# Performance work log

Measured on AMD Instinct MI355X. Metric: run time of the kernel, lower is better.

## Reference

```python
import jax, jax.numpy as jnp
import numpy as np

# Model dims
B, S, D = 4, 2048, 2048   # batch, seq, emb_dim
E, K, M = 8, 2, 1024      # num_experts, num_experts_per_tok, intermediate_dim


def setup_inputs() -> dict:
    key = jax.random.key(0)
    k0, k1, k2, k3, k4 = jax.random.split(key, 5)
    d_scale = D ** -0.5
    m_scale = M ** -0.5
    return {
        "x": jax.random.normal(k0, (B, S, D), jnp.float32),
        "w_gate": jax.random.normal(k1, (D, E), jnp.float32) * d_scale,
        "wi_0": jax.random.normal(k2, (E, D, M), jnp.float32) * d_scale,  # gate proj per expert
        "wi_1": jax.random.normal(k3, (E, D, M), jnp.float32) * d_scale,  # up proj per expert
        "wo": jax.random.normal(k4, (E, M, D), jnp.float32) * m_scale,    # down proj per expert
    }


def reference(x, w_gate, wi_0, wi_1, wo):
    b, s, d = x.shape
    e = w_gate.shape[1]
    xf = x.reshape(-1, d)                       # [T, D], T = B*S
    # --- gate logits + top-k routing ---
    logits = jnp.dot(xf, w_gate)                # [T, E]
    top_logits, top_idx = jax.lax.top_k(logits, K)    # [T, K]
    weights = jax.nn.softmax(top_logits, axis=-1)     # [T, K] router weights
    # --- sort token copies by assigned expert (dispatch) ---
    flat_idx = top_idx.reshape(-1)              # [T*K] expert id per token copy
    sort_order = jnp.argsort(flat_idx)          # [T*K] dispatch permutation
    token_ids = sort_order // K                 # source token for each sorted slot
    sorted_x = jnp.take(xf, token_ids, axis=0)  # [T*K, D] gathered activations
    group_sizes = jnp.bincount(flat_idx, length=E).astype(jnp.int32)  # tokens per expert
    # --- grouped expert GEMMs (silu-gated MLP) ---
    h0 = jax.lax.ragged_dot(sorted_x, wi_0, group_sizes)  # [T*K, M]
    h1 = jax.lax.ragged_dot(sorted_x, wi_1, group_sizes)  # [T*K, M]
    inter = jax.nn.silu(h0) * h1
    out_sorted = jax.lax.ragged_dot(inter, wo, group_sizes)  # [T*K, D]
    # --- unsort + weighted combine ---
    unsort = jnp.argsort(sort_order)
    out = jnp.take(out_sorted, unsort, axis=0).reshape(-1, K, d)  # [T, K, D]
    out = jnp.einsum("tkd,tk->td", out, weights)
    return out.reshape(b, s, d)
```

## Files before the change

### kernel.cpp

```cpp
#include <hip/hip_runtime.h>
#include <hip/hip_bf16.h>
#include <math.h>

#define T_TOK 8192
#define DIM   2048
#define NE    8
#define MDIM  1024
#define TK    16384
#define CAP   (TK + 128)
#define MAXTILES 136

typedef __attribute__((ext_vector_type(8))) short bf16x8;
typedef __attribute__((ext_vector_type(4))) float f32x4;

typedef __attribute__((address_space(3))) unsigned char* lds_ptr_t;
typedef const __attribute__((address_space(1))) unsigned char* glb_ptr_t;

__device__ __forceinline__ unsigned short f2bf(float f) {
  union { float f; unsigned u; } v; v.f = f;
  unsigned r = v.u + 0x7fffu + ((v.u >> 16) & 1u);
  return (unsigned short)(r >> 16);
}

__device__ __forceinline__ void gload_lds16(const void* g, void* l) {
  __builtin_amdgcn_global_load_lds((glb_ptr_t)g, (lds_ptr_t)l, 16, 0, 0);
}

__global__ __launch_bounds__(256) void router_kernel(
    const float* __restrict__ x, const float* __restrict__ wg,
    int* __restrict__ tok_eid, float* __restrict__ tok_w) {
  __shared__ float wgT[NE][1024];
  int tid = threadIdx.x;
  int wave = tid >> 6, lane = tid & 63;
  int t0 = blockIdx.x * 16 + wave * 4;

  double acc[4][NE];
#pragma unroll
  for (int tt = 0; tt < 4; tt++)
#pragma unroll
    for (int e = 0; e < NE; e++) acc[tt][e] = 0.0;

  for (int p = 0; p < 2; p++) {
    __syncthreads();
#pragma unroll
    for (int j = tid; j < 2048; j += 256) {
      float4 v = ((const float4*)wg)[p * 2048 + j];
      int d = j >> 1, h = (j & 1) * 4;
      wgT[h + 0][d] = v.x;
      wgT[h + 1][d] = v.y;
      wgT[h + 2][d] = v.z;
      wgT[h + 3][d] = v.w;
    }
    __syncthreads();
#pragma unroll
    for (int it = 0; it < 4; it++) {
      int dd = it * 256 + lane * 4;
      int gd = p * 1024 + dd;
      float4 wf[NE];
#pragma unroll
      for (int e = 0; e < NE; e++) wf[e] = *(const float4*)&wgT[e][dd];
#pragma unroll
      for (int tt = 0; tt < 4; tt++) {
        float4 xv = *(const float4*)(x + (size_t)(t0 + tt) * DIM + gd);
#pragma unroll
        for (int e = 0; e < NE; e++) {
          acc[tt][e] += (double)xv.x * (double)wf[e].x;
          acc[tt][e] += (double)xv.y * (double)wf[e].y;
          acc[tt][e] += (double)xv.z * (double)wf[e].z;
          acc[tt][e] += (double)xv.w * (double)wf[e].w;
        }
      }
    }
  }
#pragma unroll
  for (int tt = 0; tt < 4; tt++)
#pragma unroll
    for (int e = 0; e < NE; e++) {
      double v = acc[tt][e];
#pragma unroll
      for (int off = 32; off > 0; off >>= 1) v += __shfl_down(v, off, 64);
      acc[tt][e] = v;
    }
  if (lane == 0) {
#pragma unroll
    for (int tt = 0; tt < 4; tt++) {
      int t = t0 + tt;
      int b0 = 0; double l0 = acc[tt][0];
#pragma unroll
      for (int e = 1; e < NE; e++) { if (acc[tt][e] > l0) { l0 = acc[tt][e]; b0 = e; } }
      int b1 = -1; double l1 = -1.0e300;
#pragma unroll
      for (int e = 0; e < NE; e++) { if (e != b0 && acc[tt][e] > l1) { l1 = acc[tt][e]; b1 = e; } }
      double w0 = 1.0 / (1.0 + exp(l1 - l0));
      tok_eid[2 * t]     = b0;
      tok_eid[2 * t + 1] = b1;
      tok_w[2 * t]     = (float)w0;
      tok_w[2 * t + 1] = (float)(1.0 - w0);
    }
  }
}

__global__ __launch_bounds__(256) void plan_kernel(
    const int* __restrict__ tok_eid, int* __restrict__ offsets,
    int* __restrict__ tstart, int* __restrict__ tok_slot) {
  __shared__ int cnt[256][NE];
  __shared__ int pre[256][NE];
  __shared__ int tot[NE];
  __shared__ int off_sh[NE + 1];
  int th = threadIdx.x;
  int c[NE];
#pragma unroll
  for (int k = 0; k < NE; k++) c[k] = 0;
  for (int i = 0; i < TK / 256; i++) {
    int e = tok_eid[i * 256 + th];
#pragma unroll
    for (int k = 0; k < NE; k++) c[k] += (e == k) ? 1 : 0;
  }
#pragma unroll
  for (int k = 0; k < NE; k++) cnt[th][k] = c[k];
  __syncthreads();
  if (th < NE) {
    int run = 0;
#pragma unroll 4
    for (int i = 0; i < 256; i++) { pre[i][th] = run; run += cnt[i][th]; }
    tot[th] = run;
  }
  __syncthreads();
  if (th == 0) {
    int s = 0, ts = 0;
    for (int e = 0; e < NE; e++) {
      off_sh[e] = s; offsets[e] = s; s += tot[e];
      tstart[e] = ts; ts += (tot[e] + 127) / 128;
    }
    offsets[NE] = s; off_sh[NE] = s; tstart[NE] = ts;
  }
  __syncthreads();
  int b[NE];
#pragma unroll
  for (int k = 0; k < NE; k++) b[k] = off_sh[k] + pre[th][k];
  for (int i = 0; i < TK / 256; i++) {
    int idx = i * 256 + th;
    int e = tok_eid[idx];
    int slot = 0;
#pragma unroll
    for (int k = 0; k < NE; k++) {
      slot = (e == k) ? b[k] : slot;
      b[k] += (e == k) ? 1 : 0;
    }
    tok_slot[idx] = slot;
  }
}

__global__ __launch_bounds__(256) void dispatch_kernel(
    const float* __restrict__ x, const int* __restrict__ tok_slot,
    unsigned short* __restrict__ sorted_x) {
  int t = blockIdx.x;
  size_t s0 = (size_t)tok_slot[2 * t] * DIM;
  size_t s1 = (size_t)tok_slot[2 * t + 1] * DIM;
  const float4* xr = (const float4*)(x + (size_t)t * DIM);
#pragma unroll
  for (int i = threadIdx.x; i < DIM / 4; i += 256) {
    float4 v = xr[i];
    ushort4 b;
    b.x = f2bf(v.x); b.y = f2bf(v.y); b.z = f2bf(v.z); b.w = f2bf(v.w);
    *(ushort4*)(sorted_x + s0 + (size_t)i * 4) = b;
    *(ushort4*)(sorted_x + s1 + (size_t)i * 4) = b;
  }
}

__global__ __launch_bounds__(256) void transpose_cast_kernel(
    const float* __restrict__ in, unsigned short* __restrict__ out, int R, int C) {
  __shared__ unsigned short tile[32][33];
  int e = blockIdx.z;
  const float* inp = in + (size_t)e * R * C;
  unsigned short* outp = out + (size_t)e * R * C;
  int c0 = blockIdx.x * 32, r0 = blockIdx.y * 32;
  int tx = threadIdx.x & 31, ty = threadIdx.x >> 5;
#pragma unroll
  for (int i = 0; i < 32; i += 8)
    tile[ty + i][tx] = f2bf(inp[(size_t)(r0 + ty + i) * C + (c0 + tx)]);
  __syncthreads();
#pragma unroll
  for (int i = 0; i < 32; i += 8)
    outp[(size_t)(c0 + ty + i) * R + (r0 + tx)] = tile[tx][ty + i];
}

__global__ __launch_bounds__(256) void gemm12_kernel(
    const unsigned short* __restrict__ A, const unsigned short* __restrict__ W0t,
    const unsigned short* __restrict__ W1t, const int* __restrict__ offsets,
    const int* __restrict__ tstart, unsigned short* __restrict__ inter) {
  int bx = blockIdx.x;
  if (bx >= tstart[NE]) return;
  int e = 0;
#pragma unroll
  for (int k = 1; k < NE; k++) if (tstart[k] <= bx) e = k;
  int row0 = offsets[e], row_end = offsets[e + 1];
  int tile_r0 = row0 + (bx - tstart[e]) * 128;
  if (tile_r0 >= row_end) return;
  int col0 = blockIdx.y * 64;

  __shared__ unsigned short As[128 * 32];
  __shared__ unsigned short B0s[64 * 32];
  __shared__ unsigned short B1s[64 * 32];

  int tid = threadIdx.x;
  int wave = tid >> 6, lane = tid & 63;
  int wm = wave >> 1, wn = wave & 1;

  const unsigned short* B0 = W0t + ((size_t)e * MDIM + col0) * DIM;
  const unsigned short* B1 = W1t + ((size_t)e * MDIM + col0) * DIM;

  f32x4 acc0[4][2], acc1[4][2];
#pragma unroll
  for (int i = 0; i < 4; i++)
#pragma unroll
    for (int j = 0; j < 2; j++) {
      acc0[i][j] = (f32x4){0.f, 0.f, 0.f, 0.f};
      acc1[i][j] = (f32x4){0.f, 0.f, 0.f, 0.f};
    }

  int lrow = lane >> 2;
  int lkoff = (lane & 3) * 8;

  for (int k0 = 0; k0 < DIM; k0 += 32) {
#pragma unroll
    for (int c = 0; c < 2; c++) {
      int r = wave * 32 + c * 16 + lrow;
      gload_lds16(A + (size_t)(tile_r0 + r) * DIM + k0 + lkoff,
                  &As[(wave * 32 + c * 16) * 32]);
    }
    {
      int r = wave * 16 + lrow;
      gload_lds16(B0 + (size_t)r * DIM + k0 + lkoff, &B0s[(wave * 16) * 32]);
      gload_lds16(B1 + (size_t)r * DIM + k0 + lkoff, &B1s[(wave * 16) * 32]);
    }
    __syncthreads();
    bf16x8 af[4], b0f[2], b1f[2];
#pragma unroll
    for (int mi = 0; mi < 4; mi++)
      af[mi] = *(const bf16x8*)&As[(wm * 64 + mi * 16 + (lane & 15)) * 32 + (lane >> 4) * 8];
#pragma unroll
    for (int ni = 0; ni < 2; ni++) {
      b0f[ni] = *(const bf16x8*)&B0s[(wn * 32 + ni * 16 + (lane & 15)) * 32 + (lane >> 4) * 8];
      b1f[ni] = *(const bf16x8*)&B1s[(wn * 32 + ni * 16 + (lane & 15)) * 32 + (lane >> 4) * 8];
    }
#pragma unroll
    for (int mi = 0; mi < 4; mi++)
#pragma unroll
      for (int ni = 0; ni < 2; ni++) {
        acc0[mi][ni] = __builtin_amdgcn_mfma_f32_16x16x32_bf16(af[mi], b0f[ni], acc0[mi][ni], 0, 0, 0);
        acc1[mi][ni] = __builtin_amdgcn_mfma_f32_16x16x32_bf16(af[mi], b1f[ni], acc1[mi][ni], 0, 0, 0);
      }
    __syncthreads();
  }
#pragma unroll
  for (int mi = 0; mi < 4; mi++)
#pragma unroll
    for (int reg = 0; reg < 4; reg++) {
      int grow = tile_r0 + wm * 64 + mi * 16 + (lane >> 4) * 4 + reg;
      if (grow < row_end) {
#pragma unroll
        for (int ni = 0; ni < 2; ni++) {
          float h0 = acc0[mi][ni][reg];
          float h1 = acc1[mi][ni][reg];
          float g = h0 / (1.0f + __expf(-h0));
          int col = col0 + wn * 32 + ni * 16 + (lane & 15);
          inter[(size_t)grow * MDIM + col] = f2bf(g * h1);
        }
      }
    }
}

__global__ __launch_bounds__(256) void gemm3_kernel(
    const unsigned short* __restrict__ A, const unsigned short* __restrict__ Wot,
    const int* __restrict__ offsets, const int* __restrict__ tstart,
    float* __restrict__ out_sorted) {
  int bx = blockIdx.x;
  if (bx >= tstart[NE]) return;
  int e = 0;
#pragma unroll
  for (int k = 1; k < NE; k++) if (tstart[k] <= bx) e = k;
  int row0 = offsets[e], row_end = offsets[e + 1];
  int tile_r0 = row0 + (bx - tstart[e]) * 128;
  if (tile_r0 >= row_end) return;
  int col0 = blockIdx.y * 128;

  __shared__ unsigned short As[128 * 32];
  __shared__ unsigned short Bs[128 * 32];

  int tid = threadIdx.x;
  int wave = tid >> 6, lane = tid & 63;
  int wm = wave >> 1, wn = wave & 1;

  const unsigned short* B = Wot + ((size_t)e * DIM + col0) * MDIM;

  f32x4 acc[4][4];
#pragma unroll
  for (int i = 0; i < 4; i++)
#pragma unroll
    for (int j = 0; j < 4; j++) acc[i][j] = (f32x4){0.f, 0.f, 0.f, 0.f};

  int lrow = lane >> 2;
  int lkoff = (lane & 3) * 8;

  for (int k0 = 0; k0 < MDIM; k0 += 32) {
#pragma unroll
    for (int c = 0; c < 2; c++) {
      int r = wave * 32 + c * 16 + lrow;
      gload_lds16(A + (size_t)(tile_r0 + r) * MDIM + k0 + lkoff,
                  &As[(wave * 32 + c * 16) * 32]);
      gload_lds16(B + (size_t)r * MDIM + k0 + lkoff,
                  &Bs[(wave * 32 + c * 16) * 32]);
    }
    __syncthreads();
    bf16x8 af[4], bfr[4];
#pragma unroll
    for (int mi = 0; mi < 4; mi++)
      af[mi] = *(const bf16x8*)&As[(wm * 64 + mi * 16 + (lane & 15)) * 32 + (lane >> 4) * 8];
#pragma unroll
    for (int ni = 0; ni < 4; ni++)
      bfr[ni] = *(const bf16x8*)&Bs[(wn * 64 + ni * 16 + (lane & 15)) * 32 + (lane >> 4) * 8];
#pragma unroll
    for (int mi = 0; mi < 4; mi++)
#pragma unroll
      for (int ni = 0; ni < 4; ni++)
        acc[mi][ni] = __builtin_amdgcn_mfma_f32_16x16x32_bf16(af[mi], bfr[ni], acc[mi][ni], 0, 0, 0);
    __syncthreads();
  }
#pragma unroll
  for (int mi = 0; mi < 4; mi++)
#pragma unroll
    for (int reg = 0; reg < 4; reg++) {
      int grow = tile_r0 + wm * 64 + mi * 16 + (lane >> 4) * 4 + reg;
      if (grow < row_end) {
        float* orow = out_sorted + (size_t)grow * DIM + col0 + wn * 64 + (lane & 15);
#pragma unroll
        for (int ni = 0; ni < 4; ni++)
          orow[ni * 16] = acc[mi][ni][reg];
      }
    }
}

__global__ __launch_bounds__(256) void combine_kernel(
    const float* __restrict__ os, const int* __restrict__ tok_slot,
    const float* __restrict__ tok_w, float* __restrict__ out) {
  int t = blockIdx.x * 4 + (threadIdx.x >> 6);
  int lane = threadIdx.x & 63;
  int s0 = tok_slot[2 * t], s1 = tok_slot[2 * t + 1];
  float w0 = tok_w[2 * t], w1 = tok_w[2 * t + 1];
  const float4* a = (const float4*)(os + (size_t)s0 * DIM);
  const float4* b = (const float4*)(os + (size_t)s1 * DIM);
  float4* o = (float4*)(out + (size_t)t * DIM);
#pragma unroll
  for (int i = lane; i < DIM / 4; i += 64) {
    float4 va = a[i], vb = b[i];
    float4 r;
    r.x = w0 * va.x + w1 * vb.x;
    r.y = w0 * va.y + w1 * vb.y;
    r.z = w0 * va.z + w1 * vb.z;
    r.w = w0 * va.w + w1 * vb.w;
    o[i] = r;
  }
}

extern "C" void kernel_launch(void* const* d_in, const int* in_sizes, int n_in,
                              void* d_out, int out_size, void* d_ws, size_t ws_size,
                              hipStream_t stream) {
  const float* x   = (const float*)d_in[0];
  const float* wg  = (const float*)d_in[1];
  const float* wi0 = (const float*)d_in[2];
  const float* wi1 = (const float*)d_in[3];
  const float* wo  = (const float*)d_in[4];
  float* out = (float*)d_out;

  char* ws = (char*)d_ws;
  size_t off = 0;
  auto alloc = [&](size_t bytes) -> void* {
    void* p = ws + off;
    off = (off + bytes + 255) & ~(size_t)255;
    return p;
  };
  int*   offsets  = (int*)alloc((NE + 1) * 4);
  int*   tstart   = (int*)alloc((NE + 1) * 4);
  int*   tok_eid  = (int*)alloc((size_t)2 * T_TOK * 4);
  float* tok_w    = (float*)alloc((size_t)2 * T_TOK * 4);
  int*   tok_slot = (int*)alloc((size_t)2 * T_TOK * 4);
  unsigned short* inter    = (unsigned short*)alloc((size_t)CAP * MDIM * 2);
  unsigned short* sorted_x = (unsigned short*)alloc((size_t)CAP * DIM * 2);
  unsigned short* W0t      = (unsigned short*)alloc((size_t)NE * MDIM * DIM * 2);
  unsigned short* W1t      = (unsigned short*)alloc((size_t)NE * MDIM * DIM * 2);
  unsigned short* Wot      = (unsigned short*)alloc((size_t)NE * DIM * MDIM * 2);
  float* out_sorted = (float*)sorted_x;

  router_kernel<<<T_TOK / 16, 256, 0, stream>>>(x, wg, tok_eid, tok_w);
  plan_kernel<<<1, 256, 0, stream>>>(tok_eid, offsets, tstart, tok_slot);
  dispatch_kernel<<<T_TOK, 256, 0, stream>>>(x, tok_slot, sorted_x);
  transpose_cast_kernel<<<dim3(MDIM / 32, DIM / 32, NE), 256, 0, stream>>>(wi0, W0t, DIM, MDIM);
  transpose_cast_kernel<<<dim3(MDIM / 32, DIM / 32, NE), 256, 0, stream>>>(wi1, W1t, DIM, MDIM);
  transpose_cast_kernel<<<dim3(DIM / 32, MDIM / 32, NE), 256, 0, stream>>>(wo, Wot, MDIM, DIM);

  gemm12_kernel<<<dim3(MAXTILES, MDIM / 64, 1), 256, 0, stream>>>(
      sorted_x, W0t, W1t, offsets, tstart, inter);
  gemm3_kernel<<<dim3(MAXTILES, DIM / 128, 1), 256, 0, stream>>>(
      inter, Wot, offsets, tstart, out_sorted);
  combine_kernel<<<T_TOK / 4, 256, 0, stream>>>(out_sorted, tok_slot, tok_w, out);
}
```

Before: 681.1 us.

## Rewrite grouped GEMMs with 256-row tiles, swizzled double-buffered LDS and interleaved loads

```diff
diff --git a/kernel.cpp b/kernel.cpp
--- a/kernel.cpp
+++ b/kernel.cpp
@@ -7,8 +7,8 @@
 #define NE    8
 #define MDIM  1024
 #define TK    16384
-#define CAP   (TK + 128)
-#define MAXTILES 136
+#define CAP   (TK + 256)
+#define MAXT  72
 
 typedef __attribute__((ext_vector_type(8))) short bf16x8;
 typedef __attribute__((ext_vector_type(4))) float f32x4;
@@ -24,6 +24,24 @@
 
 __device__ __forceinline__ void gload_lds16(const void* g, void* l) {
   __builtin_amdgcn_global_load_lds((glb_ptr_t)g, (lds_ptr_t)l, 16, 0, 0);
+}
+
+#define VM_FENCE(n) asm volatile("s_waitcnt vmcnt(" #n ")" ::: "memory")
+#define BARRIER() __builtin_amdgcn_s_barrier()
+
+__device__ __forceinline__ void stage_unit(const unsigned short* __restrict__ src,
+                                           int ld, unsigned char* lds, int tid) {
+#pragma unroll
+  for (int j = 0; j < 2; j++) {
+    int idx = j * 512 + tid;
+    int row = idx >> 3;
+    int gslot = (idx & 7) ^ (row & 7);
+    gload_lds16(src + (size_t)row * ld + gslot * 8, lds + ((idx & ~63) << 4));
+  }
+}
+
+__device__ __forceinline__ bf16x8 ldsfrag(const unsigned char* base, int row, int kb) {
+  return *(const bf16x8*)(base + row * 128 + (kb ^ ((row & 7) << 4)));
 }
 
 __global__ __launch_bounds__(256) void router_kernel(
@@ -130,7 +148,7 @@
     int s = 0, ts = 0;
     for (int e = 0; e < NE; e++) {
       off_sh[e] = s; offsets[e] = s; s += tot[e];
-      tstart[e] = ts; ts += (tot[e] + 127) / 128;
+      tstart[e] = ts; ts += (tot[e] + 255) / 256;
     }
     offsets[NE] = s; off_sh[NE] = s; tstart[NE] = ts;
   }
@@ -185,160 +203,284 @@
     outp[(size_t)(c0 + ty + i) * R + (r0 + tx)] = tile[tx][ty + i];
 }
 
-__global__ __launch_bounds__(256) void gemm12_kernel(
+__global__ __launch_bounds__(512, 2) void gemm12_kernel(
     const unsigned short* __restrict__ A, const unsigned short* __restrict__ W0t,
     const unsigned short* __restrict__ W1t, const int* __restrict__ offsets,
     const int* __restrict__ tstart, unsigned short* __restrict__ inter) {
+  extern __shared__ unsigned char smem[];
   int bx = blockIdx.x;
   if (bx >= tstart[NE]) return;
   int e = 0;
 #pragma unroll
   for (int k = 1; k < NE; k++) if (tstart[k] <= bx) e = k;
   int row0 = offsets[e], row_end = offsets[e + 1];
-  int tile_r0 = row0 + (bx - tstart[e]) * 128;
+  int tile_r0 = row0 + (bx - tstart[e]) * 256;
   if (tile_r0 >= row_end) return;
-  int col0 = blockIdx.y * 64;
-
-  __shared__ unsigned short As[128 * 32];
-  __shared__ unsigned short B0s[64 * 32];
-  __shared__ unsigned short B1s[64 * 32];
+  int colb = blockIdx.y * 128;
 
   int tid = threadIdx.x;
   int wave = tid >> 6, lane = tid & 63;
-  int wm = wave >> 1, wn = wave & 1;
-
-  const unsigned short* B0 = W0t + ((size_t)e * MDIM + col0) * DIM;
-  const unsigned short* B1 = W1t + ((size_t)e * MDIM + col0) * DIM;
-
-  f32x4 acc0[4][2], acc1[4][2];
-#pragma unroll
-  for (int i = 0; i < 4; i++)
+  int wm = wave >> 2, wn = wave & 3;
+  int l15 = lane & 15, grp16 = (lane >> 4) * 16;
+
+  const unsigned short* Ab = A + (size_t)tile_r0 * DIM;
+  const unsigned short* B0b = W0t + ((size_t)e * MDIM + colb) * DIM;
+  const unsigned short* B1b = W1t + ((size_t)e * MDIM + colb) * DIM;
+
+  f32x4 acc0[8][2], acc1[8][2];
+#pragma unroll
+  for (int i = 0; i < 8; i++)
 #pragma unroll
     for (int j = 0; j < 2; j++) {
       acc0[i][j] = (f32x4){0.f, 0.f, 0.f, 0.f};
       acc1[i][j] = (f32x4){0.f, 0.f, 0.f, 0.f};
     }
-
-  int lrow = lane >> 2;
-  int lkoff = (lane & 3) * 8;
-
-  for (int k0 = 0; k0 < DIM; k0 += 32) {
-#pragma unroll
-    for (int c = 0; c < 2; c++) {
-      int r = wave * 32 + c * 16 + lrow;
-      gload_lds16(A + (size_t)(tile_r0 + r) * DIM + k0 + lkoff,
-                  &As[(wave * 32 + c * 16) * 32]);
-    }
-    {
-      int r = wave * 16 + lrow;
-      gload_lds16(B0 + (size_t)r * DIM + k0 + lkoff, &B0s[(wave * 16) * 32]);
-      gload_lds16(B1 + (size_t)r * DIM + k0 + lkoff, &B1s[(wave * 16) * 32]);
-    }
-    __syncthreads();
-    bf16x8 af[4], b0f[2], b1f[2];
+  bf16x8 af[4][2], b0f[2][2], b1f[2][2];
+
+  stage_unit(Ab, DIM, smem + 0, tid);
+  stage_unit(B0b, DIM, smem + 32768, tid);
+  stage_unit(B1b, DIM, smem + 49152, tid);
+  stage_unit(Ab + (size_t)128 * DIM, DIM, smem + 16384, tid);
+  VM_FENCE(4);
+  BARRIER();
+
+  for (int t = 0; t < 32; t++) {
+    unsigned char* S = smem + (t & 1) * 65536;
+    unsigned char* P = smem + ((t & 1) ^ 1) * 65536;
+    int kn = (t < 31 ? t + 1 : t) * 64;
+#pragma unroll
+    for (int mi = 0; mi < 4; mi++) {
+      int r = wm * 64 + mi * 16 + l15;
+#pragma unroll
+      for (int ks = 0; ks < 2; ks++) af[mi][ks] = ldsfrag(S, r, ks * 64 + grp16);
+    }
+#pragma unroll
+    for (int ni = 0; ni < 2; ni++) {
+      int r = wn * 32 + ni * 16 + l15;
+#pragma unroll
+      for (int ks = 0; ks < 2; ks++) b0f[ni][ks] = ldsfrag(S + 32768, r, ks * 64 + grp16);
+    }
+    stage_unit(Ab + kn, DIM, P, tid);
+    BARRIER();
+    __builtin_amdgcn_s_setprio(1);
+#pragma unroll
+    for (int ks = 0; ks < 2; ks++)
+#pragma unroll
+      for (int mi = 0; mi < 4; mi++)
+#pragma unroll
+        for (int ni = 0; ni < 2; ni++)
+          acc0[mi][ni] = __builtin_amdgcn_mfma_f32_16x16x32_bf16(af[mi][ks], b0f[ni][ks], acc0[mi][ni], 0, 0, 0);
+    __builtin_amdgcn_s_setprio(0);
+    VM_FENCE(4);
+    BARRIER();
+#pragma unroll
+    for (int ni = 0; ni < 2; ni++) {
+      int r = wn * 32 + ni * 16 + l15;
+#pragma unroll
+      for (int ks = 0; ks < 2; ks++) b1f[ni][ks] = ldsfrag(S + 49152, r, ks * 64 + grp16);
+    }
+    stage_unit(B0b + kn, DIM, P + 32768, tid);
+    BARRIER();
+    __builtin_amdgcn_s_setprio(1);
+#pragma unroll
+    for (int ks = 0; ks < 2; ks++)
+#pragma unroll
+      for (int mi = 0; mi < 4; mi++)
+#pragma unroll
+        for (int ni = 0; ni < 2; ni++)
+          acc1[mi][ni] = __builtin_amdgcn_mfma_f32_16x16x32_bf16(af[mi][ks], b1f[ni][ks], acc1[mi][ni], 0, 0, 0);
+    __builtin_amdgcn_s_setprio(0);
+    VM_FENCE(4);
+    BARRIER();
+#pragma unroll
+    for (int mi = 0; mi < 4; mi++) {
+      int r = 128 + wm * 64 + mi * 16 + l15;
+#pragma unroll
+      for (int ks = 0; ks < 2; ks++) af[mi][ks] = ldsfrag(S, r, ks * 64 + grp16);
+    }
+    stage_unit(B1b + kn, DIM, P + 49152, tid);
+    BARRIER();
+    __builtin_amdgcn_s_setprio(1);
+#pragma unroll
+    for (int ks = 0; ks < 2; ks++)
+#pragma unroll
+      for (int mi = 0; mi < 4; mi++)
+#pragma unroll
+        for (int ni = 0; ni < 2; ni++)
+          acc0[4 + mi][ni] = __builtin_amdgcn_mfma_f32_16x16x32_bf16(af[mi][ks], b0f[ni][ks], acc0[4 + mi][ni], 0, 0, 0);
+    __builtin_amdgcn_s_setprio(0);
+    BARRIER();
+    stage_unit(Ab + (size_t)128 * DIM + kn, DIM, P + 16384, tid);
+    BARRIER();
+    __builtin_amdgcn_s_setprio(1);
+#pragma unroll
+    for (int ks = 0; ks < 2; ks++)
+#pragma unroll
+      for (int mi = 0; mi < 4; mi++)
+#pragma unroll
+        for (int ni = 0; ni < 2; ni++)
+          acc1[4 + mi][ni] = __builtin_amdgcn_mfma_f32_16x16x32_bf16(af[mi][ks], b1f[ni][ks], acc1[4 + mi][ni], 0, 0, 0);
+    __builtin_amdgcn_s_setprio(0);
+    VM_FENCE(4);
+    BARRIER();
+  }
+  VM_FENCE(0);
+
+#pragma unroll
+  for (int half = 0; half < 2; half++)
 #pragma unroll
     for (int mi = 0; mi < 4; mi++)
-      af[mi] = *(const bf16x8*)&As[(wm * 64 + mi * 16 + (lane & 15)) * 32 + (lane >> 4) * 8];
-#pragma unroll
-    for (int ni = 0; ni < 2; ni++) {
-      b0f[ni] = *(const bf16x8*)&B0s[(wn * 32 + ni * 16 + (lane & 15)) * 32 + (lane >> 4) * 8];
-      b1f[ni] = *(const bf16x8*)&B1s[(wn * 32 + ni * 16 + (lane & 15)) * 32 + (lane >> 4) * 8];
-    }
-#pragma unroll
-    for (int mi = 0; mi < 4; mi++)
-#pragma unroll
-      for (int ni = 0; ni < 2; ni++) {
-        acc0[mi][ni] = __builtin_amdgcn_mfma_f32_16x16x32_bf16(af[mi], b0f[ni], acc0[mi][ni], 0, 0, 0);
-        acc1[mi][ni] = __builtin_amdgcn_mfma_f32_16x16x32_bf16(af[mi], b1f[ni], acc1[mi][ni], 0, 0, 0);
-      }
-    __syncthreads();
-  }
-#pragma unroll
-  for (int mi = 0; mi < 4; mi++)
-#pragma unroll
-    for (int reg = 0; reg < 4; reg++) {
-      int grow = tile_r0 + wm * 64 + mi * 16 + (lane >> 4) * 4 + reg;
-      if (grow < row_end) {
-#pragma unroll
-        for (int ni = 0; ni < 2; ni++) {
-          float h0 = acc0[mi][ni][reg];
-          float h1 = acc1[mi][ni][reg];
-          float g = h0 / (1.0f + __expf(-h0));
-          int col = col0 + wn * 32 + ni * 16 + (lane & 15);
-          inter[(size_t)grow * MDIM + col] = f2bf(g * h1);
+#pragma unroll
+      for (int reg = 0; reg < 4; reg++) {
+        int grow = tile_r0 + half * 128 + wm * 64 + mi * 16 + (lane >> 4) * 4 + reg;
+        if (grow < row_end) {
+#pragma unroll
+          for (int ni = 0; ni < 2; ni++) {
+            float h0 = acc0[half * 4 + mi][ni][reg];
+            float h1 = acc1[half * 4 + mi][ni][reg];
+            float g = h0 / (1.0f + __expf(-h0));
+            inter[(size_t)grow * MDIM + colb + wn * 32 + ni * 16 + l15] = f2bf(g * h1);
+          }
         }
       }
-    }
-}
-
-__global__ __launch_bounds__(256) void gemm3_kernel(
+}
+
+__global__ __launch_bounds__(512, 2) void gemm3_kernel(
     const unsigned short* __restrict__ A, const unsigned short* __restrict__ Wot,
     const int* __restrict__ offsets, const int* __restrict__ tstart,
     float* __restrict__ out_sorted) {
+  extern __shared__ unsigned char smem[];
   int bx = blockIdx.x;
   if (bx >= tstart[NE]) return;
   int e = 0;
 #pragma unroll
   for (int k = 1; k < NE; k++) if (tstart[k] <= bx) e = k;
   int row0 = offsets[e], row_end = offsets[e + 1];
-  int tile_r0 = row0 + (bx - tstart[e]) * 128;
+  int tile_r0 = row0 + (bx - tstart[e]) * 256;
   if (tile_r0 >= row_end) return;
-  int col0 = blockIdx.y * 128;
-
-  __shared__ unsigned short As[128 * 32];
-  __shared__ unsigned short Bs[128 * 32];
+  int col0 = blockIdx.y * 256;
 
   int tid = threadIdx.x;
   int wave = tid >> 6, lane = tid & 63;
-  int wm = wave >> 1, wn = wave & 1;
-
-  const unsigned short* B = Wot + ((size_t)e * DIM + col0) * MDIM;
-
-  f32x4 acc[4][4];
-#pragma unroll
-  for (int i = 0; i < 4; i++)
+  int wm = wave >> 2, wn = wave & 3;
+  int l15 = lane & 15, grp16 = (lane >> 4) * 16;
+
+  const unsigned short* Ab = A + (size_t)tile_r0 * MDIM;
+  const unsigned short* Bb = Wot + ((size_t)e * DIM + col0) * MDIM;
+
+  f32x4 acc[8][4];
+#pragma unroll
+  for (int i = 0; i < 8; i++)
 #pragma unroll
     for (int j = 0; j < 4; j++) acc[i][j] = (f32x4){0.f, 0.f, 0.f, 0.f};
-
-  int lrow = lane >> 2;
-  int lkoff = (lane & 3) * 8;
-
-  for (int k0 = 0; k0 < MDIM; k0 += 32) {
-#pragma unroll
-    for (int c = 0; c < 2; c++) {
-      int r = wave * 32 + c * 16 + lrow;
-      gload_lds16(A + (size_t)(tile_r0 + r) * MDIM + k0 + lkoff,
-                  &As[(wave * 32 + c * 16) * 32]);
-      gload_lds16(B + (size_t)r * MDIM + k0 + lkoff,
-                  &Bs[(wave * 32 + c * 16) * 32]);
-    }
-    __syncthreads();
-    bf16x8 af[4], bfr[4];
+  bf16x8 af[4][2], bfr[4][2];
+
+  stage_unit(Ab, MDIM, smem + 0, tid);
+  stage_unit(Bb, MDIM, smem + 32768, tid);
+  stage_unit(Bb + (size_t)128 * MDIM, MDIM, smem + 49152, tid);
+  stage_unit(Ab + (size_t)128 * MDIM, MDIM, smem + 16384, tid);
+  VM_FENCE(4);
+  BARRIER();
+
+  for (int t = 0; t < 16; t++) {
+    unsigned char* S = smem + (t & 1) * 65536;
+    unsigned char* P = smem + ((t & 1) ^ 1) * 65536;
+    int kn = (t < 15 ? t + 1 : t) * 64;
+#pragma unroll
+    for (int mi = 0; mi < 4; mi++) {
+      int r = wm * 64 + mi * 16 + l15;
+#pragma unroll
+      for (int ks = 0; ks < 2; ks++) af[mi][ks] = ldsfrag(S, r, ks * 64 + grp16);
+    }
+#pragma unroll
+    for (int ni = 0; ni < 2; ni++) {
+      int r = wn * 32 + ni * 16 + l15;
+#pragma unroll
+      for (int ks = 0; ks < 2; ks++) bfr[ni][ks] = ldsfrag(S + 32768, r, ks * 64 + grp16);
+    }
+    stage_unit(Ab + kn, MDIM, P, tid);
+    BARRIER();
+    __builtin_amdgcn_s_setprio(1);
+#pragma unroll
+    for (int ks = 0; ks < 2; ks++)
+#pragma unroll
+      for (int mi = 0; mi < 4; mi++)
+#pragma unroll
+        for (int ni = 0; ni < 2; ni++)
+          acc[mi][ni] = __builtin_amdgcn_mfma_f32_16x16x32_bf16(af[mi][ks], bfr[ni][ks], acc[mi][ni], 0, 0, 0);
+    __builtin_amdgcn_s_setprio(0);
+    VM_FENCE(4);
+    BARRIER();
+#pragma unroll
+    for (int ni = 0; ni < 2; ni++) {
+      int r = 128 + wn * 32 + ni * 16 + l15;
+#pragma unroll
+      for (int ks = 0; ks < 2; ks++) bfr[2 + ni][ks] = ldsfrag(S + 32768, r, ks * 64 + grp16);
+    }
+    stage_unit(Bb + kn, MDIM, P + 32768, tid);
+    BARRIER();
+    __builtin_amdgcn_s_setprio(1);
+#pragma unroll
+    for (int ks = 0; ks < 2; ks++)
+#pragma unroll
+      for (int mi = 0; mi < 4; mi++)
+#pragma unroll
+        for (int ni = 0; ni < 2; ni++)
+          acc[mi][2 + ni] = __builtin_amdgcn_mfma_f32_16x16x32_bf16(af[mi][ks], bfr[2 + ni][ks], acc[mi][2 + ni], 0, 0, 0);
+    __builtin_amdgcn_s_setprio(0);
+    VM_FENCE(4);
+    BARRIER();
+#pragma unroll
+    for (int mi = 0; mi < 4; mi++) {
+      int r = 128 + wm * 64 + mi * 16 + l15;
+#pragma unroll
+      for (int ks = 0; ks < 2; ks++) af[mi][ks] = ldsfrag(S, r, ks * 64 + grp16);
+    }
+    stage_unit(Bb + (size_t)128 * MDIM + kn, MDIM, P + 49152, tid);
+    BARRIER();
+    __builtin_amdgcn_s_setprio(1);
+#pragma unroll
+    for (int ks = 0; ks < 2; ks++)
+#pragma unroll
+      for (int mi = 0; mi < 4; mi++)
+#pragma unroll
+        for (int ni = 0; ni < 2; ni++)
+          acc[4 + mi][ni] = __builtin_amdgcn_mfma_f32_16x16x32_bf16(af[mi][ks], bfr[ni][ks], acc[4 + mi][ni], 0, 0, 0);
+    __builtin_amdgcn_s_setprio(0);
+    BARRIER();
+    stage_unit(Ab + (size_t)128 * MDIM + kn, MDIM, P + 16384, tid);
+    BARRIER();
+    __builtin_amdgcn_s_setprio(1);
+#pragma unroll
+    for (int ks = 0; ks < 2; ks++)
+#pragma unroll
+      for (int mi = 0; mi < 4; mi++)
+#pragma unroll
+        for (int ni = 0; ni < 2; ni++)
+          acc[4 + mi][2 + ni] = __builtin_amdgcn_mfma_f32_16x16x32_bf16(af[mi][ks], bfr[2 + ni][ks], acc[4 + mi][2 + ni], 0, 0, 0);
+    __builtin_amdgcn_s_setprio(0);
+    VM_FENCE(4);
+    BARRIER();
+  }
+  VM_FENCE(0);
+
+#pragma unroll
+  for (int mh = 0; mh < 2; mh++)
 #pragma unroll
     for (int mi = 0; mi < 4; mi++)
-      af[mi] = *(const bf16x8*)&As[(wm * 64 + mi * 16 + (lane & 15)) * 32 + (lane >> 4) * 8];
-#pragma unroll
-    for (int ni = 0; ni < 4; ni++)
-      bfr[ni] = *(const bf16x8*)&Bs[(wn * 64 + ni * 16 + (lane & 15)) * 32 + (lane >> 4) * 8];
-#pragma unroll
-    for (int mi = 0; mi < 4; mi++)
-#pragma unroll
-      for (int ni = 0; ni < 4; ni++)
-        acc[mi][ni] = __builtin_amdgcn_mfma_f32_16x16x32_bf16(af[mi], bfr[ni], acc[mi][ni], 0, 0, 0);
-    __syncthreads();
-  }
-#pragma unroll
-  for (int mi = 0; mi < 4; mi++)
-#pragma unroll
-    for (int reg = 0; reg < 4; reg++) {
-      int grow = tile_r0 + wm * 64 + mi * 16 + (lane >> 4) * 4 + reg;
-      if (grow < row_end) {
-        float* orow = out_sorted + (size_t)grow * DIM + col0 + wn * 64 + (lane & 15);
-#pragma unroll
-        for (int ni = 0; ni < 4; ni++)
-          orow[ni * 16] = acc[mi][ni][reg];
+#pragma unroll
+      for (int reg = 0; reg < 4; reg++) {
+        int grow = tile_r0 + mh * 128 + wm * 64 + mi * 16 + (lane >> 4) * 4 + reg;
+        if (grow < row_end) {
+#pragma unroll
+          for (int nh = 0; nh < 2; nh++) {
+            float* orow = out_sorted + (size_t)grow * DIM + col0 + nh * 128 + wn * 32 + l15;
+#pragma unroll
+            for (int ni = 0; ni < 2; ni++)
+              orow[ni * 16] = acc[mh * 4 + mi][nh * 2 + ni][reg];
+          }
+        }
       }
-    }
 }
 
 __global__ __launch_bounds__(256) void combine_kernel(
@@ -372,6 +514,11 @@
   const float* wi1 = (const float*)d_in[3];
   const float* wo  = (const float*)d_in[4];
   float* out = (float*)d_out;
+
+  (void)hipFuncSetAttribute(reinterpret_cast<const void*>(gemm12_kernel),
+                            hipFuncAttributeMaxDynamicSharedMemorySize, 131072);
+  (void)hipFuncSetAttribute(reinterpret_cast<const void*>(gemm3_kernel),
+                            hipFuncAttributeMaxDynamicSharedMemorySize, 131072);
 
   char* ws = (char*)d_ws;
   size_t off = 0;
@@ -399,9 +546,9 @@
   transpose_cast_kernel<<<dim3(MDIM / 32, DIM / 32, NE), 256, 0, stream>>>(wi1, W1t, DIM, MDIM);
   transpose_cast_kernel<<<dim3(DIM / 32, MDIM / 32, NE), 256, 0, stream>>>(wo, Wot, MDIM, DIM);
 
-  gemm12_kernel<<<dim3(MAXTILES, MDIM / 64, 1), 256, 0, stream>>>(
+  gemm12_kernel<<<dim3(MAXT, MDIM / 128, 1), 512, 131072, stream>>>(
       sorted_x, W0t, W1t, offsets, tstart, inter);
-  gemm3_kernel<<<dim3(MAXTILES, DIM / 128, 1), 256, 0, stream>>>(
+  gemm3_kernel<<<dim3(MAXT, DIM / 256, 1), 512, 131072, stream>>>(
       inter, Wot, offsets, tstart, out_sorted);
   combine_kernel<<<T_TOK / 4, 256, 0, stream>>>(out_sorted, tok_slot, tok_w, out);
 }
```

Result: faster. 614.7 us (-9.7%).
